# Kernel optimization log

Hardware: AMD Instinct MI355X
Metric: run time of the kernel (lower is better)

The kernel has to match this reference:

```python
import jax, jax.numpy as jnp
import numpy as np


def setup_inputs() -> dict:
    key = jax.random.key(0)
    ks = jax.random.split(key, 8)
    B, C, W, H = 4, 256, 64, 64
    Cq = C // 8
    return {
        "input": jax.random.normal(ks[0], (B, C, W, H), dtype=jnp.float32),
        "Wf": jax.random.normal(ks[1], (Cq, C), dtype=jnp.float32) * 0.05,
        "bf": jax.random.normal(ks[2], (Cq,), dtype=jnp.float32) * 0.05,
        "Wg": jax.random.normal(ks[3], (Cq, C), dtype=jnp.float32) * 0.05,
        "bg": jax.random.normal(ks[4], (Cq,), dtype=jnp.float32) * 0.05,
        "Wh": jax.random.normal(ks[5], (C, C), dtype=jnp.float32) * 0.05,
        "bh": jax.random.normal(ks[6], (C,), dtype=jnp.float32) * 0.05,
        "gamma": jax.random.normal(ks[7], (1,), dtype=jnp.float32),
    }


def reference(input, Wf, bf, Wg, bg, Wh, bh, gamma):
    # input: [B, C, W, H]; SAGAN self-attention over N = W*H spatial tokens.
    B, C, W, H = input.shape
    N = W * H
    x = input.reshape(B, C, N)
    # 1x1 Conv1d == per-token linear projection over channels.
    f = jnp.einsum('oc,bcn->bon', Wf, x) + bf[None, :, None]  # [B, C/8, N]
    g = jnp.einsum('oc,bcn->bon', Wg, x) + bg[None, :, None]  # [B, C/8, N]
    h = jnp.einsum('oc,bcn->bon', Wh, x) + bh[None, :, None]  # [B, C,   N]
    # s = f^T g -> [B, N, N]; softmax over last dim (columns / g-tokens).
    s = jnp.einsum('bon,bom->bnm', f, g)
    attention = jax.nn.softmax(s, axis=-1)
    # out = h @ attention^T : out[b,c,m] = sum_n h[b,c,n] * attention[b,m,n]
    out = jnp.einsum('bcn,bmn->bcm', h, attention)
    out = out.reshape(B, C, W, H)
    return gamma[0] * out + input
```

## Files before the change

kernel.cpp:

```cpp
#include <hip/hip_runtime.h>

typedef _Float16 half8 __attribute__((ext_vector_type(8)));
typedef _Float16 half4 __attribute__((ext_vector_type(4)));
typedef unsigned int uintx2 __attribute__((ext_vector_type(2)));
typedef unsigned int uintx4 __attribute__((ext_vector_type(4)));
typedef float floatx16 __attribute__((ext_vector_type(16)));

#define MFMA_F16(A, B, C) __builtin_amdgcn_mfma_f32_32x32x16_f16(A, B, C, 0, 0, 0)

constexpr int Bn = 4;
constexpr int Cc = 256;
constexpr int Cq = 32;
constexpr int Nn = 4096;
constexpr float LOG2E = 1.44269504088896340736f;


__device__ inline floatx16 zero16() {
  floatx16 z;
#pragma unroll
  for (int i = 0; i < 16; ++i) z[i] = 0.f;
  return z;
}

__device__ inline unsigned int pkrtz(float a, float b) {
  return __builtin_bit_cast(unsigned int, __builtin_amdgcn_cvt_pkrtz(a, b));
}

__global__ __launch_bounds__(256) void k_wconv(
    const float* __restrict__ Wf, const float* __restrict__ Wg,
    const float* __restrict__ Wh, _Float16* __restrict__ Wfh,
    _Float16* __restrict__ Wgh, _Float16* __restrict__ Whh) {
  int e = (blockIdx.x * 256 + threadIdx.x) * 4;
  const float* src;
  _Float16* dst;
  float sc = 1.f;
  if (e < 8192) { src = Wf + e; dst = Wfh + e; sc = LOG2E; }
  else if (e < 16384) { src = Wg + (e - 8192); dst = Wgh + (e - 8192); }
  else { src = Wh + (e - 16384); dst = Whh + (e - 16384); }
  float4 v = *(const float4*)src;
  half4 o;
  o[0] = (_Float16)(v.x * sc); o[1] = (_Float16)(v.y * sc);
  o[2] = (_Float16)(v.z * sc); o[3] = (_Float16)(v.w * sc);
  *(half4*)dst = o;
}

__global__ __launch_bounds__(512) void k_proj(
    const float* __restrict__ x,
    const _Float16* __restrict__ Wfh, const float* __restrict__ bf,
    const _Float16* __restrict__ Wgh, const float* __restrict__ bg,
    const _Float16* __restrict__ Whh, const float* __restrict__ bh,
    _Float16* __restrict__ Q, _Float16* __restrict__ K4,
    _Float16* __restrict__ V8) {
  __shared__ float xs[32][260];
  int tid = threadIdx.x;
  int w = tid >> 6, lane = tid & 63;
  int ml = lane & 31, h = lane >> 5;
  int b = blockIdx.x >> 7, nt = blockIdx.x & 127;
  int n0 = nt * 32;

  {
    int c = tid >> 3;
    int nl = (tid & 7) * 4;
    const float* xp = x + (size_t)b * Cc * Nn + n0 + nl;
#pragma unroll
    for (int pass = 0; pass < 4; ++pass) {
      int cc = c + pass * 64;
      float4 v = *(const float4*)(xp + (size_t)cc * Nn);
      xs[nl + 0][cc] = v.x;
      xs[nl + 1][cc] = v.y;
      xs[nl + 2][cc] = v.z;
      xs[nl + 3][cc] = v.w;
    }
  }
  __syncthreads();

  half8 bfr[16];
#pragma unroll
  for (int kc = 0; kc < 16; ++kc) {
    const float* xp = &xs[ml][kc * 16 + h * 8];
    half8 f;
#pragma unroll
    for (int j = 0; j < 8; ++j) f[j] = (_Float16)xp[j];
    bfr[kc] = f;
  }

  for (int t = w; t < 10; t += 8) {
    const _Float16* W;
    const float* bias;
    float bscale = 1.f;
    int o0 = 0;
    if (t == 0) { W = Wfh; bias = bf; bscale = LOG2E; }
    else if (t == 1) { W = Wgh; bias = bg; }
    else { W = Whh + (size_t)(t - 2) * 32 * Cc; bias = bh + (t - 2) * 32; o0 = (t - 2) * 32; }

    floatx16 acc = zero16();
    const _Float16* wp = W + (size_t)ml * Cc + h * 8;
#pragma unroll
    for (int kc = 0; kc < 16; ++kc) {
      half8 a = *(const half8*)(wp + kc * 16);
      acc = MFMA_F16(a, bfr[kc], acc);
    }

    if (t == 0) {
      _Float16* op = Q + ((size_t)b * Nn + n0 + ml) * Cq;
#pragma unroll
      for (int qd = 0; qd < 4; ++qd) {
        float4 bq = *(const float4*)(bias + 8 * qd + 4 * h);
        const float* bqp = (const float*)&bq;
#pragma unroll
        for (int i = 0; i < 4; ++i) {
          int crow = i + 8 * qd + 4 * h;
          op[crow] = (_Float16)(acc[4 * qd + i] + bqp[i] * bscale);
        }
      }
    } else if (t == 1) {
#pragma unroll
      for (int qd = 0; qd < 4; ++qd) {
        float4 bq = *(const float4*)(bias + 8 * qd + 4 * h);
        const float* bqp = (const float*)&bq;
#pragma unroll
        for (int i = 0; i < 4; ++i) {
          int crow = i + 8 * qd + 4 * h;
          K4[(((size_t)b * 4 + (crow >> 3)) * Nn + n0 + ml) * 8 + (crow & 7)] =
              (_Float16)(acc[4 * qd + i] + bqp[i]);
        }
      }
    } else {
      size_t nb = (size_t)((n0 + ml) >> 3);
      _Float16* op = V8 + (((size_t)b * 512 + nb) * 256) * 8 + (ml & 7);
#pragma unroll
      for (int qd = 0; qd < 4; ++qd) {
        float4 bq = *(const float4*)(bias + 8 * qd + 4 * h);
        const float* bqp = (const float*)&bq;
#pragma unroll
        for (int i = 0; i < 4; ++i) {
          int crow = i + 8 * qd + 4 * h;
          op[(size_t)(o0 + crow) * 8] = (_Float16)(acc[4 * qd + i] + bqp[i]);
        }
      }
    }
  }
}

__global__ __launch_bounds__(512) void k_rowmax(const _Float16* __restrict__ Q,
                                                const _Float16* __restrict__ K4,
                                                float* __restrict__ M) {
  __shared__ float red[8][32];
  int tid = threadIdx.x, w = tid >> 6, lane = tid & 63;
  int ml = lane & 31, h = lane >> 5;
  int b = blockIdx.x >> 7, mt = blockIdx.x & 127;
  int m0 = mt * 32;
  const _Float16* qp = Q + ((size_t)b * Nn + m0 + ml) * Cq + h * 8;
  half8 qb0 = *(const half8*)(qp);
  half8 qb1 = *(const half8*)(qp + 16);
  const _Float16* kp0 = K4 + (((size_t)b * 4 + h) * Nn + w * 512 + ml) * 8;
  const _Float16* kp1 = K4 + (((size_t)b * 4 + 2 + h) * Nn + w * 512 + ml) * 8;
  float mx = -3.0e38f;
  for (int t = 0; t < 16; ++t) {
    floatx16 s = zero16();
    half8 k0 = *(const half8*)(kp0 + (size_t)t * 32 * 8);
    half8 k1 = *(const half8*)(kp1 + (size_t)t * 32 * 8);
    s = MFMA_F16(k0, qb0, s);
    s = MFMA_F16(k1, qb1, s);
#pragma unroll
    for (int i = 0; i < 16; ++i) mx = fmaxf(mx, s[i]);
  }
  mx = fmaxf(mx, __shfl_xor(mx, 32, 64));
  if (h == 0) red[w][ml] = mx;
  __syncthreads();
  if (tid < 32) {
    float m2 = red[0][tid];
#pragma unroll
    for (int i = 1; i < 8; ++i) m2 = fmaxf(m2, red[i][tid]);
    M[(size_t)b * Nn + m0 + tid] = m2;
  }
}

__device__ inline void otree_write(float2* dst, const floatx16* o) {
#pragma unroll
  for (int cb = 0; cb < 8; ++cb)
#pragma unroll
    for (int rp = 0; rp < 8; ++rp)
      dst[(cb * 8 + rp) * 64] = make_float2(o[cb][2 * rp], o[cb][2 * rp + 1]);
}

__device__ inline void otree_add(const float2* src, floatx16* o) {
#pragma unroll
  for (int cb = 0; cb < 8; ++cb)
#pragma unroll
    for (int rp = 0; rp < 8; ++rp) {
      float2 v = src[(cb * 8 + rp) * 64];
      o[cb][2 * rp] += v.x;
      o[cb][2 * rp + 1] += v.y;
    }
}

__global__ __launch_bounds__(512, 2) void k_attn(
    const _Float16* __restrict__ Q, const _Float16* __restrict__ K4,
    const _Float16* __restrict__ V8, const float* __restrict__ M,
    const float* __restrict__ xin, const float* __restrict__ gamma,
    float* __restrict__ out) {
  __shared__ float Ored[4 * 8192];
  __shared__ float lred[8][32];
  int tid = threadIdx.x, w = tid >> 6, lane = tid & 63;
  int ml = lane & 31, h = lane >> 5;
  int bx = blockIdx.x;
  int mt = bx & 127, b = bx >> 7;
  int m0 = mt * 32;

  const _Float16* qp = Q + ((size_t)b * Nn + m0 + ml) * Cq + h * 8;
  half8 qb0 = *(const half8*)(qp);
  half8 qb1 = *(const half8*)(qp + 16);
  float Mv = M[(size_t)b * Nn + m0 + ml];
  float g = gamma[0];
  float lacc = 0.f;

  const _Float16* k4b0 = K4 + (((size_t)b * 4 + h) * Nn + w * 32 + ml) * 8;
  const _Float16* k4b1 = K4 + (((size_t)b * 4 + 2 + h) * Nn + w * 32 + ml) * 8;
  const _Float16* v8b = V8 + (((size_t)b * 512 + w * 4 + h) * 256 + ml) * 8;

  floatx16 o[8];
#pragma unroll
  for (int i = 0; i < 8; ++i) o[i] = zero16();

  half8 k0 = *(const half8*)(k4b0);
  half8 k1 = *(const half8*)(k4b1);

  for (int it = 0; it < 16; ++it) {
    floatx16 s = zero16();
    s = MFMA_F16(k0, qb0, s);
    s = MFMA_F16(k1, qb1, s);
    k0 = *(const half8*)(k4b0 + (size_t)(it + 1) * 2048);
    k1 = *(const half8*)(k4b1 + (size_t)(it + 1) * 2048);
    float p[16];
#pragma unroll
    for (int i = 0; i < 16; ++i) p[i] = __builtin_amdgcn_exp2f(s[i] - Mv);
#pragma unroll
    for (int i = 0; i < 16; ++i) lacc += p[i];
    unsigned int c0 = pkrtz(p[0], p[1]),  c1 = pkrtz(p[2], p[3]);
    unsigned int c2 = pkrtz(p[4], p[5]),  c3 = pkrtz(p[6], p[7]);
    unsigned int c4 = pkrtz(p[8], p[9]),  c5 = pkrtz(p[10], p[11]);
    unsigned int c6 = pkrtz(p[12], p[13]), c7 = pkrtz(p[14], p[15]);
    uintx2 t02 = __builtin_amdgcn_permlane32_swap(c0, c2, false, false);
    uintx2 t13 = __builtin_amdgcn_permlane32_swap(c1, c3, false, false);
    uintx2 t46 = __builtin_amdgcn_permlane32_swap(c4, c6, false, false);
    uintx2 t57 = __builtin_amdgcn_permlane32_swap(c5, c7, false, false);
    uintx4 f0v = {t02.x, t13.x, t02.y, t13.y};
    uintx4 f1v = {t46.x, t57.x, t46.y, t57.y};
    half8 pf0 = __builtin_bit_cast(half8, f0v);
    half8 pf1 = __builtin_bit_cast(half8, f1v);
    const _Float16* vp = v8b + (size_t)it * 65536;
#pragma unroll
    for (int cb = 0; cb < 8; ++cb) {
      half8 vf0 = *(const half8*)(vp + cb * 256);
      o[cb] = MFMA_F16(vf0, pf0, o[cb]);
    }
#pragma unroll
    for (int cb = 0; cb < 8; ++cb) {
      half8 vf1 = *(const half8*)(vp + 4096 + cb * 256);
      o[cb] = MFMA_F16(vf1, pf1, o[cb]);
    }
  }

  lacc += __shfl_xor(lacc, 32, 64);
  if (h == 0) lred[w][ml] = lacc;

  float2* Ored2 = (float2*)Ored;
  int lofs = h * 32 + ml;
  if (w >= 4) otree_write(Ored2 + (w - 4) * 4096 + lofs, o);
  __syncthreads();
  if (w < 4) otree_add(Ored2 + w * 4096 + lofs, o);
  __syncthreads();
  if (w == 2 || w == 3) otree_write(Ored2 + (w - 2) * 4096 + lofs, o);
  __syncthreads();
  if (w < 2) otree_add(Ored2 + w * 4096 + lofs, o);
  __syncthreads();
  if (w == 1) otree_write(Ored2 + lofs, o);
  __syncthreads();
  if (w == 0) { otree_add(Ored2 + lofs, o); otree_write(Ored2 + lofs, o); }
  __syncthreads();

  float lv = 0.f;
#pragma unroll
  for (int i = 0; i < 8; ++i) lv += lred[i][ml];
  float scale = g / lv;
  const float2* src = Ored2 + lofs;
  size_t obase = ((size_t)b * 256 + w * 32) * (size_t)Nn + m0 + ml;
#pragma unroll
  for (int rp = 0; rp < 8; ++rp) {
    float2 v = src[(w * 8 + rp) * 64];
    int r = 2 * rp;
    int cA = (r & 3) + 8 * (r >> 2) + 4 * h;
    size_t oa = obase + (size_t)cA * Nn;
    out[oa] = scale * v.x + xin[oa];
    out[oa + Nn] = scale * v.y + xin[oa + Nn];
  }
}

extern "C" void kernel_launch(void* const* d_in, const int* in_sizes, int n_in,
                              void* d_out, int out_size, void* d_ws,
                              size_t ws_size, hipStream_t stream) {
  const float* x = (const float*)d_in[0];
  const float* Wf = (const float*)d_in[1];
  const float* bf = (const float*)d_in[2];
  const float* Wg = (const float*)d_in[3];
  const float* bg = (const float*)d_in[4];
  const float* Wh = (const float*)d_in[5];
  const float* bh = (const float*)d_in[6];
  const float* gamma = (const float*)d_in[7];
  float* out = (float*)d_out;

  char* ws = (char*)d_ws;
  _Float16* Q  = (_Float16*)(ws);
  _Float16* K4 = (_Float16*)(ws + 1048576);
  _Float16* V8 = (_Float16*)(ws + 2097152);
  float*    M  = (float*)   (ws + 10485760);
  _Float16* Wfh = (_Float16*)(ws + 10551296);
  _Float16* Wgh = (_Float16*)(ws + 10567680);
  _Float16* Whh = (_Float16*)(ws + 10584064);

  k_wconv<<<dim3(80), dim3(256), 0, stream>>>(Wf, Wg, Wh, Wfh, Wgh, Whh);
  k_proj<<<dim3(512), dim3(512), 0, stream>>>(x, Wfh, bf, Wgh, bg, Whh, bh, Q, K4, V8);
  k_rowmax<<<dim3(512), dim3(512), 0, stream>>>(Q, K4, M);
  k_attn<<<dim3(512), dim3(512), 0, stream>>>(Q, K4, V8, M, x, gamma, out);
}
```

Measured before the change: 167.8 us.

## Coalesce V8 stores via LDS transpose and halve attention reduction LDS

The projection kernel now stages the V tile in a per-wave shared-memory buffer and writes V8 with 16-byte vector stores, replacing scattered 2-byte global stores. The attention kernel's cross-wave output reduction buffer shrinks from 128KB to 64KB. The reduction tree is reordered into more serialized stages so only two partial buffers are needed. This trades two extra barrier stages for lower LDS use, which may raise occupancy under the 2-blocks-per-CU launch bound.

```diff
diff --git a/kernel.cpp b/kernel.cpp
--- a/kernel.cpp
+++ b/kernel.cpp
@@ -52,6 +52,7 @@
     _Float16* __restrict__ Q, _Float16* __restrict__ K4,
     _Float16* __restrict__ V8) {
   __shared__ float xs[32][260];
+  __shared__ _Float16 vtr[8][1280];
   int tid = threadIdx.x;
   int w = tid >> 6, lane = tid & 63;
   int ml = lane & 31, h = lane >> 5;
@@ -126,8 +127,7 @@
         }
       }
     } else {
-      size_t nb = (size_t)((n0 + ml) >> 3);
-      _Float16* op = V8 + (((size_t)b * 512 + nb) * 256) * 8 + (ml & 7);
+      _Float16* vs = vtr[w];
 #pragma unroll
       for (int qd = 0; qd < 4; ++qd) {
         float4 bq = *(const float4*)(bias + 8 * qd + 4 * h);
@@ -135,8 +135,15 @@
 #pragma unroll
         for (int i = 0; i < 4; ++i) {
           int crow = i + 8 * qd + 4 * h;
-          op[(size_t)(o0 + crow) * 8] = (_Float16)(acc[4 * qd + i] + bqp[i]);
+          vs[crow * 40 + ml] = (_Float16)(acc[4 * qd + i] + bqp[i]);
         }
+      }
+      const _Float16* rs = vtr[w] + ml * 40;
+#pragma unroll
+      for (int r = 0; r < 2; ++r) {
+        int tg = h * 2 + r;
+        half8 vv = *(const half8*)(rs + tg * 8);
+        *(half8*)(V8 + (((size_t)b * 512 + (n0 >> 3) + tg) * 256 + o0 + ml) * 8) = vv;
       }
     }
   }
@@ -200,7 +207,7 @@
     const _Float16* __restrict__ V8, const float* __restrict__ M,
     const float* __restrict__ xin, const float* __restrict__ gamma,
     float* __restrict__ out) {
-  __shared__ float Ored[4 * 8192];
+  __shared__ float Ored[2 * 8192];
   __shared__ float lred[8][32];
   int tid = threadIdx.x, w = tid >> 6, lane = tid & 63;
   int ml = lane & 31, h = lane >> 5;
@@ -267,13 +274,23 @@
 
   float2* Ored2 = (float2*)Ored;
   int lofs = h * 32 + ml;
-  if (w >= 4) otree_write(Ored2 + (w - 4) * 4096 + lofs, o);
-  __syncthreads();
-  if (w < 4) otree_add(Ored2 + w * 4096 + lofs, o);
-  __syncthreads();
-  if (w == 2 || w == 3) otree_write(Ored2 + (w - 2) * 4096 + lofs, o);
-  __syncthreads();
-  if (w < 2) otree_add(Ored2 + w * 4096 + lofs, o);
+  if (w == 4) otree_write(Ored2 + lofs, o);
+  if (w == 5) otree_write(Ored2 + 4096 + lofs, o);
+  __syncthreads();
+  if (w == 0) otree_add(Ored2 + lofs, o);
+  if (w == 1) otree_add(Ored2 + 4096 + lofs, o);
+  __syncthreads();
+  if (w == 6) otree_write(Ored2 + lofs, o);
+  if (w == 7) otree_write(Ored2 + 4096 + lofs, o);
+  __syncthreads();
+  if (w == 2) otree_add(Ored2 + lofs, o);
+  if (w == 3) otree_add(Ored2 + 4096 + lofs, o);
+  __syncthreads();
+  if (w == 2) otree_write(Ored2 + lofs, o);
+  if (w == 3) otree_write(Ored2 + 4096 + lofs, o);
+  __syncthreads();
+  if (w == 0) otree_add(Ored2 + lofs, o);
+  if (w == 1) otree_add(Ored2 + 4096 + lofs, o);
   __syncthreads();
   if (w == 1) otree_write(Ored2 + lofs, o);
   __syncthreads();
```

Measured after the change: 163.5 us. 1.03x faster.

## Split attention block into two query halves and stage V stores through LDS

Applied to the files above, without the earlier changes.

The attention kernel now has each block handle 64 query rows. Two groups of four waves each own a 32-row half, and each wave sweeps twice as many key tiles. The launch grid drops to 256 blocks, and the reduction tree shrinks to two levels per half, cutting barriers and LDS traffic per output. Separately, the projection kernel transposes V through a small LDS buffer so it can write contiguous half8 vectors instead of strided scalar stores. The trade-off is fewer blocks on the GPU (256 on a 256-CU part, possibly lowering occupancy and latency hiding) and longer per-wave loops.

```diff
diff --git a/kernel.cpp b/kernel.cpp
--- a/kernel.cpp
+++ b/kernel.cpp
@@ -52,6 +52,7 @@
     _Float16* __restrict__ Q, _Float16* __restrict__ K4,
     _Float16* __restrict__ V8) {
   __shared__ float xs[32][260];
+  __shared__ _Float16 vtr[8][1280];
   int tid = threadIdx.x;
   int w = tid >> 6, lane = tid & 63;
   int ml = lane & 31, h = lane >> 5;
@@ -126,8 +127,7 @@
         }
       }
     } else {
-      size_t nb = (size_t)((n0 + ml) >> 3);
-      _Float16* op = V8 + (((size_t)b * 512 + nb) * 256) * 8 + (ml & 7);
+      _Float16* vs = vtr[w];
 #pragma unroll
       for (int qd = 0; qd < 4; ++qd) {
         float4 bq = *(const float4*)(bias + 8 * qd + 4 * h);
@@ -135,8 +135,15 @@
 #pragma unroll
         for (int i = 0; i < 4; ++i) {
           int crow = i + 8 * qd + 4 * h;
-          op[(size_t)(o0 + crow) * 8] = (_Float16)(acc[4 * qd + i] + bqp[i]);
+          vs[crow * 40 + ml] = (_Float16)(acc[4 * qd + i] + bqp[i]);
         }
+      }
+      const _Float16* rs = vtr[w] + ml * 40;
+#pragma unroll
+      for (int r = 0; r < 2; ++r) {
+        int tg = h * 2 + r;
+        half8 vv = *(const half8*)(rs + tg * 8);
+        *(half8*)(V8 + (((size_t)b * 512 + (n0 >> 3) + tg) * 256 + o0 + ml) * 8) = vv;
       }
     }
   }
@@ -204,9 +211,11 @@
   __shared__ float lred[8][32];
   int tid = threadIdx.x, w = tid >> 6, lane = tid & 63;
   int ml = lane & 31, h = lane >> 5;
+  int mh = w >> 2, nw = w & 3;
   int bx = blockIdx.x;
-  int mt = bx & 127, b = bx >> 7;
-  int m0 = mt * 32;
+  int mt = bx & 63, b = bx >> 6;
+  int mb = mt * 64;
+  int m0 = mb + mh * 32;
 
   const _Float16* qp = Q + ((size_t)b * Nn + m0 + ml) * Cq + h * 8;
   half8 qb0 = *(const half8*)(qp);
@@ -215,9 +224,9 @@
   float g = gamma[0];
   float lacc = 0.f;
 
-  const _Float16* k4b0 = K4 + (((size_t)b * 4 + h) * Nn + w * 32 + ml) * 8;
-  const _Float16* k4b1 = K4 + (((size_t)b * 4 + 2 + h) * Nn + w * 32 + ml) * 8;
-  const _Float16* v8b = V8 + (((size_t)b * 512 + w * 4 + h) * 256 + ml) * 8;
+  const _Float16* k4b0 = K4 + (((size_t)b * 4 + h) * Nn + nw * 32 + ml) * 8;
+  const _Float16* k4b1 = K4 + (((size_t)b * 4 + 2 + h) * Nn + nw * 32 + ml) * 8;
+  const _Float16* v8b = V8 + (((size_t)b * 512 + nw * 4 + h) * 256 + ml) * 8;
 
   floatx16 o[8];
 #pragma unroll
@@ -226,12 +235,12 @@
   half8 k0 = *(const half8*)(k4b0);
   half8 k1 = *(const half8*)(k4b1);
 
-  for (int it = 0; it < 16; ++it) {
+  for (int it = 0; it < 32; ++it) {
     floatx16 s = zero16();
     s = MFMA_F16(k0, qb0, s);
     s = MFMA_F16(k1, qb1, s);
-    k0 = *(const half8*)(k4b0 + (size_t)(it + 1) * 2048);
-    k1 = *(const half8*)(k4b1 + (size_t)(it + 1) * 2048);
+    k0 = *(const half8*)(k4b0 + (size_t)(it + 1) * 1024);
+    k1 = *(const half8*)(k4b1 + (size_t)(it + 1) * 1024);
     float p[16];
 #pragma unroll
     for (int i = 0; i < 16; ++i) p[i] = __builtin_amdgcn_exp2f(s[i] - Mv);
@@ -249,7 +258,7 @@
     uintx4 f1v = {t46.x, t57.x, t46.y, t57.y};
     half8 pf0 = __builtin_bit_cast(half8, f0v);
     half8 pf1 = __builtin_bit_cast(half8, f1v);
-    const _Float16* vp = v8b + (size_t)it * 65536;
+    const _Float16* vp = v8b + (size_t)it * 32768;
 #pragma unroll
     for (int cb = 0; cb < 8; ++cb) {
       half8 vf0 = *(const half8*)(vp + cb * 256);
@@ -267,33 +276,39 @@
 
   float2* Ored2 = (float2*)Ored;
   int lofs = h * 32 + ml;
-  if (w >= 4) otree_write(Ored2 + (w - 4) * 4096 + lofs, o);
-  __syncthreads();
-  if (w < 4) otree_add(Ored2 + w * 4096 + lofs, o);
-  __syncthreads();
-  if (w == 2 || w == 3) otree_write(Ored2 + (w - 2) * 4096 + lofs, o);
-  __syncthreads();
-  if (w < 2) otree_add(Ored2 + w * 4096 + lofs, o);
-  __syncthreads();
-  if (w == 1) otree_write(Ored2 + lofs, o);
-  __syncthreads();
-  if (w == 0) { otree_add(Ored2 + lofs, o); otree_write(Ored2 + lofs, o); }
-  __syncthreads();
-
-  float lv = 0.f;
-#pragma unroll
-  for (int i = 0; i < 8; ++i) lv += lred[i][ml];
-  float scale = g / lv;
-  const float2* src = Ored2 + lofs;
-  size_t obase = ((size_t)b * 256 + w * 32) * (size_t)Nn + m0 + ml;
+  float2* rg0 = Ored2 + (size_t)(mh * 2) * 4096 + lofs;
+  float2* rg1 = Ored2 + (size_t)(mh * 2 + 1) * 4096 + lofs;
+  if (nw == 2) otree_write(rg0, o);
+  if (nw == 3) otree_write(rg1, o);
+  __syncthreads();
+  if (nw == 0) otree_add(rg0, o);
+  if (nw == 1) otree_add(rg1, o);
+  __syncthreads();
+  if (nw == 1) otree_write(rg1, o);
+  __syncthreads();
+  if (nw == 0) { otree_add(rg1, o); otree_write(rg0, o); }
+  __syncthreads();
+
+  float lv0 = lred[0][ml] + lred[1][ml] + lred[2][ml] + lred[3][ml];
+  float lv1 = lred[4][ml] + lred[5][ml] + lred[6][ml] + lred[7][ml];
+  float sc0 = g / lv0;
+  float sc1 = g / lv1;
+  const float2* src0 = Ored2 + lofs;
+  const float2* src1 = Ored2 + (size_t)2 * 4096 + lofs;
+  size_t obase0 = ((size_t)b * 256 + w * 32) * (size_t)Nn + mb + ml;
+  size_t obase1 = obase0 + 32;
 #pragma unroll
   for (int rp = 0; rp < 8; ++rp) {
-    float2 v = src[(w * 8 + rp) * 64];
     int r = 2 * rp;
     int cA = (r & 3) + 8 * (r >> 2) + 4 * h;
-    size_t oa = obase + (size_t)cA * Nn;
-    out[oa] = scale * v.x + xin[oa];
-    out[oa + Nn] = scale * v.y + xin[oa + Nn];
+    size_t oa0 = obase0 + (size_t)cA * Nn;
+    size_t oa1 = obase1 + (size_t)cA * Nn;
+    float2 v0 = src0[(w * 8 + rp) * 64];
+    float2 v1 = src1[(w * 8 + rp) * 64];
+    out[oa0] = sc0 * v0.x + xin[oa0];
+    out[oa0 + Nn] = sc0 * v0.y + xin[oa0 + Nn];
+    out[oa1] = sc1 * v1.x + xin[oa1];
+    out[oa1 + Nn] = sc1 * v1.y + xin[oa1 + Nn];
   }
 }
 
@@ -322,5 +337,5 @@
   k_wconv<<<dim3(80), dim3(256), 0, stream>>>(Wf, Wg, Wh, Wfh, Wgh, Whh);
   k_proj<<<dim3(512), dim3(512), 0, stream>>>(x, Wfh, bf, Wgh, bg, Whh, bh, Q, K4, V8);
   k_rowmax<<<dim3(512), dim3(512), 0, stream>>>(Q, K4, M);
-  k_attn<<<dim3(512), dim3(512), 0, stream>>>(Q, K4, V8, M, x, gamma, out);
-}
+  k_attn<<<dim3(256), dim3(512), 0, stream>>>(Q, K4, V8, M, x, gamma, out);
+}
```

Result: faster. 157.0 us (-6.5%).
